# Kernel tuning notes

Measured on AMD Instinct MI355X. Metric: run time of the kernel, lower is better.

Reference implementation:

```python
import jax, jax.numpy as jnp
import numpy as np

N_NODES = 50000


def sage_conv(x, src, dst, Wl, bl, Wr):
    # mean-aggregate neighbor features: message from src -> dst
    msg = x[src]                                            # [E, d]
    agg = jax.ops.segment_sum(msg, dst, num_segments=N_NODES)
    deg = jax.ops.segment_sum(jnp.ones((src.shape[0],), x.dtype), dst,
                              num_segments=N_NODES)
    mean = agg / jnp.clip(deg, 1.0)[:, None]                # [N, d]
    # PyG SAGEConv: lin_l(mean) + lin_r(x); lin_l has bias, lin_r does not
    return mean @ Wl.T + bl + x @ Wr.T


def setup_inputs() -> dict:
    key = jax.random.key(0)
    ks = jax.random.split(key, 10)
    d_in, d_h = 128, 256
    E = 800000
    x = jax.random.normal(ks[0], (N_NODES, d_in), jnp.float32)
    edge_index = jax.random.randint(ks[1], (2, E), 0, N_NODES, jnp.int32)
    s = 0.05
    return {
        "x": x,
        "edge_index": edge_index,
        "W1_l": jax.random.normal(ks[2], (d_h, d_in), jnp.float32) * s,
        "b1": jax.random.normal(ks[3], (d_h,), jnp.float32) * s,
        "W1_r": jax.random.normal(ks[4], (d_h, d_in), jnp.float32) * s,
        "W2_l": jax.random.normal(ks[5], (d_h, d_h), jnp.float32) * s,
        "b2": jax.random.normal(ks[6], (d_h,), jnp.float32) * s,
        "W2_r": jax.random.normal(ks[7], (d_h, d_h), jnp.float32) * s,
        "head_w": jax.random.normal(ks[8], (1, d_h), jnp.float32) * s,
        "head_b": jax.random.normal(ks[9], (1,), jnp.float32) * s,
    }


def reference(x, edge_index, W1_l, b1, W1_r, W2_l, b2, W2_r, head_w, head_b):
    src, dst = edge_index[0], edge_index[1]
    h = jax.nn.relu(sage_conv(x, src, dst, W1_l, b1, W1_r))
    # dropout is identity in eval mode
    h = jax.nn.relu(sage_conv(h, src, dst, W2_l, b2, W2_r))
    out = h @ head_w.T + head_b                              # [N, 1]
    return out[:, 0]                                         # [N]
```

## Files before the change

kernel.cpp:

```cpp
#include <hip/hip_runtime.h>
#include <hip/hip_bf16.h>
#include <hip/hip_fp8.h>

#define D_IN 128
#define D_H  256

typedef __attribute__((ext_vector_type(8))) short short8;
typedef __attribute__((ext_vector_type(4))) float floatx4;

__device__ __forceinline__ unsigned short f2bf(float f) {
    __hip_bfloat16 h = __float2bfloat16(f);
    return *reinterpret_cast<unsigned short*>(&h);
}
__device__ __forceinline__ float bf2f(unsigned short s) {
    union { unsigned int u; float f; } v;
    v.u = ((unsigned int)s) << 16;
    return v.f;
}
__device__ __forceinline__ unsigned char f2fp8(float f) {
    __hip_fp8_e4m3 t(f);
    return (unsigned char)t.__x;
}

__global__ void hist_conv_k(const int* __restrict__ dst, int* __restrict__ deg,
                            int* __restrict__ rank, int E,
                            const float* __restrict__ x, unsigned short* __restrict__ xb,
                            unsigned char* __restrict__ xb8, int nx4,
                            const float* __restrict__ w1l, unsigned short* __restrict__ w1lb,
                            const float* __restrict__ w1r, unsigned short* __restrict__ w1rb, int nw14,
                            const float* __restrict__ w2l, unsigned short* __restrict__ w2lb,
                            const float* __restrict__ w2r, unsigned short* __restrict__ w2rb, int nw24) {
    if (blockIdx.x < 512) {
        for (int e = blockIdx.x * 256 + threadIdx.x; e < E; e += 512 * 256)
            rank[e] = atomicAdd(&deg[dst[e]], 1);
        return;
    }
    int i = (blockIdx.x - 512) * 256 + threadIdx.x;
    if (i < nx4) {
        float4 v = ((const float4*)x)[i];
        ushort4 u;
        u.x = f2bf(v.x); u.y = f2bf(v.y); u.z = f2bf(v.z); u.w = f2bf(v.w);
        ((ushort4*)xb)[i] = u;
        uchar4 c;
        c.x = f2fp8(v.x); c.y = f2fp8(v.y); c.z = f2fp8(v.z); c.w = f2fp8(v.w);
        ((uchar4*)xb8)[i] = c;
        return;
    }
    i -= nx4;
    const float* s; unsigned short* d; int k;
    if (i < nw14) { s = w1l; d = w1lb; k = i; }
    else {
        i -= nw14;
        if (i < nw14) { s = w1r; d = w1rb; k = i; }
        else {
            i -= nw14;
            if (i < nw24) { s = w2l; d = w2lb; k = i; }
            else {
                i -= nw24;
                if (i >= nw24) return;
                s = w2r; d = w2rb; k = i;
            }
        }
    }
    float4 v = ((const float4*)s)[k];
    ushort4 u;
    u.x = f2bf(v.x); u.y = f2bf(v.y); u.z = f2bf(v.z); u.w = f2bf(v.w);
    ((ushort4*)d)[k] = u;
}

__global__ __launch_bounds__(256) void scan_part_k(const int* __restrict__ deg,
                                                   int* __restrict__ bsum, int n) {
    const int b = blockIdx.x, tid = threadIdx.x;
    const int base = b * 2048;
    const int lim = min(base + 2048, n);
    int s = 0;
    for (int i = base + tid; i < lim; i += 256) s += deg[i];
    __shared__ int red[256];
    red[tid] = s; __syncthreads();
    for (int off = 128; off > 0; off >>= 1) {
        if (tid < off) red[tid] += red[tid + off];
        __syncthreads();
    }
    if (tid == 0) bsum[b] = red[0];
}

__global__ __launch_bounds__(256) void scan_final_k(const int* __restrict__ deg,
                                                    const int* __restrict__ bsum,
                                                    int* __restrict__ row_ptr,
                                                    int n, int E) {
    const int b = blockIdx.x, tid = threadIdx.x;
    const int base = b * 2048;
    __shared__ int buf[2048];
    __shared__ int ts[256];
    __shared__ int blk_prefix;
    if (tid == 0) {
        int p = 0;
        for (int i = 0; i < b; ++i) p += bsum[i];
        blk_prefix = p;
    }
    for (int i = tid; i < 2048; i += 256)
        buf[i] = (base + i < n) ? deg[base + i] : 0;
    __syncthreads();
    int local[8];
    int s = 0;
#pragma unroll
    for (int j = 0; j < 8; ++j) { local[j] = s; s += buf[tid * 8 + j]; }
    ts[tid] = s; __syncthreads();
    for (int off = 1; off < 256; off <<= 1) {
        int v = (tid >= off) ? ts[tid - off] : 0;
        __syncthreads();
        ts[tid] += v;
        __syncthreads();
    }
    const int prefix = blk_prefix + ((tid == 0) ? 0 : ts[tid - 1]);
#pragma unroll
    for (int j = 0; j < 8; ++j) {
        int idx = base + tid * 8 + j;
        if (idx < n) row_ptr[idx] = prefix + local[j];
    }
    if (b == 0 && tid == 0) row_ptr[n] = E;
}

__global__ void scatter_k(const int* __restrict__ src, const int* __restrict__ dst,
                          const int* __restrict__ rank, const int* __restrict__ row_ptr,
                          int* __restrict__ col, int E) {
    for (int e = blockIdx.x * blockDim.x + threadIdx.x; e < E; e += gridDim.x * blockDim.x)
        col[row_ptr[dst[e]] + rank[e]] = src[e];
}

template <int UNP>
__device__ __forceinline__ int agg1_stage(const unsigned char* __restrict__ X8,
                                          const int* __restrict__ col,
                                          int j, int e, int sel, int l32, float* acc) {
    for (; j + 2 * UNP <= e; j += 2 * UNP) {
        int c0[UNP], c1[UNP];
#pragma unroll
        for (int u = 0; u < UNP; ++u) { c0[u] = col[j + 2 * u]; c1[u] = col[j + 2 * u + 1]; }
        unsigned int vals[UNP];
#pragma unroll
        for (int u = 0; u < UNP; ++u) {
            const int cs = sel ? c1[u] : c0[u];
            vals[u] = *(const unsigned int*)(X8 + (size_t)cs * 128 + l32 * 4);
        }
#pragma unroll
        for (int u = 0; u < UNP; ++u) {
            __hip_fp8x4_e4m3 p;
            p.__x = vals[u];
            float4 f = (float4)p;
            acc[0] += f.x; acc[1] += f.y; acc[2] += f.z; acc[3] += f.w;
        }
    }
    return j;
}

__global__ __launch_bounds__(256) void aggregate1_k(
    const unsigned char* __restrict__ X8, const int* __restrict__ col,
    const int* __restrict__ rp, unsigned short* __restrict__ out, int Mnodes) {
    int node = __builtin_amdgcn_readfirstlane((blockIdx.x << 2) + (threadIdx.x >> 6));
    if (node >= Mnodes) return;
    const int lane = threadIdx.x & 63;
    const int sel = lane >> 5;
    const int l32 = lane & 31;
    const int s = rp[node], e = rp[node + 1];
    float acc[4] = {0.f, 0.f, 0.f, 0.f};

    int j = s;
    j = agg1_stage<4>(X8, col, j, e, sel, l32, acc);
    j = agg1_stage<2>(X8, col, j, e, sel, l32, acc);
    j = agg1_stage<1>(X8, col, j, e, sel, l32, acc);
    if (j < e) {
        const int c0 = col[j];
        if (sel == 0) {
            unsigned int v = *(const unsigned int*)(X8 + (size_t)c0 * 128 + l32 * 4);
            __hip_fp8x4_e4m3 p;
            p.__x = v;
            float4 f = (float4)p;
            acc[0] += f.x; acc[1] += f.y; acc[2] += f.z; acc[3] += f.w;
        }
    }
#pragma unroll
    for (int k = 0; k < 4; ++k) acc[k] += __shfl_xor(acc[k], 32, 64);
    const float inv = 1.f / fmaxf((float)(e - s), 1.f);
    if (sel == 0) {
        ushort4 o;
        o.x = f2bf(acc[0] * inv); o.y = f2bf(acc[1] * inv);
        o.z = f2bf(acc[2] * inv); o.w = f2bf(acc[3] * inv);
        *(ushort4*)(out + (size_t)node * 128 + l32 * 4) = o;
    }
}

template <int UN>
__device__ __forceinline__ int agg_stage_fp8(const unsigned char* __restrict__ X8,
                                             const int* __restrict__ col,
                                             int j, int e, int lane, float* acc) {
    for (; j + UN <= e; j += UN) {
        int cs[UN];
#pragma unroll
        for (int u = 0; u < UN; ++u) cs[u] = col[j + u];
        unsigned int vals[UN];
#pragma unroll
        for (int u = 0; u < UN; ++u)
            vals[u] = *(const unsigned int*)(X8 + (size_t)cs[u] * 256 + lane * 4);
#pragma unroll
        for (int u = 0; u < UN; ++u) {
            __hip_fp8x4_e4m3 p;
            p.__x = vals[u];
            float4 f = (float4)p;
            acc[0] += f.x; acc[1] += f.y; acc[2] += f.z; acc[3] += f.w;
        }
    }
    return j;
}

__global__ __launch_bounds__(256) void aggregate2_k(
    const unsigned char* __restrict__ X8, const int* __restrict__ col,
    const int* __restrict__ rp, unsigned short* __restrict__ out, int Mnodes) {
    int node = __builtin_amdgcn_readfirstlane((blockIdx.x << 2) + (threadIdx.x >> 6));
    if (node >= Mnodes) return;
    const int lane = threadIdx.x & 63;
    const int s = rp[node], e = rp[node + 1];
    float acc[4] = {0.f, 0.f, 0.f, 0.f};

    int j = s;
    j = agg_stage_fp8<8>(X8, col, j, e, lane, acc);
    j = agg_stage_fp8<4>(X8, col, j, e, lane, acc);
    j = agg_stage_fp8<2>(X8, col, j, e, lane, acc);
    j = agg_stage_fp8<1>(X8, col, j, e, lane, acc);

    const float inv = 1.f / fmaxf((float)(e - s), 1.f);
    ushort4 o;
    o.x = f2bf(acc[0] * inv); o.y = f2bf(acc[1] * inv);
    o.z = f2bf(acc[2] * inv); o.w = f2bf(acc[3] * inv);
    *(ushort4*)(out + (size_t)node * 256 + lane * 4) = o;
}

template <int K, bool HEAD>
__global__ __launch_bounds__(256, 2) void gemm_mfma_k(
    const unsigned short* __restrict__ A1, const unsigned short* __restrict__ W1,
    const unsigned short* __restrict__ A2, const unsigned short* __restrict__ W2,
    const float* __restrict__ bias, unsigned short* __restrict__ Hout,
    unsigned char* __restrict__ Hout8,
    const float* __restrict__ hw, const float* __restrict__ hb,
    float* __restrict__ out, int M) {
    __shared__ __align__(16) unsigned short sA[128 * 40];
    __shared__ __align__(16) unsigned short sB[256 * 40];
    __shared__ float head_acc[128];

    constexpr int NCK = K / 32;
    constexpr int NC = 2 * NCK;

    const int tid = threadIdx.x;
    const int wave = tid >> 6;
    const int lane = tid & 63;
    const int c = lane & 15;
    const int q = lane >> 4;
    const int m0 = blockIdx.x * 128;

    if (HEAD && tid < 128) head_acc[tid] = 0.f;

    floatx4 acc[8][4];
#pragma unroll
    for (int mi = 0; mi < 8; ++mi)
#pragma unroll
        for (int ni = 0; ni < 4; ++ni) acc[mi][ni] = (floatx4){0.f, 0.f, 0.f, 0.f};

    const int arow = tid >> 1;
    const int aseg = (tid & 1) * 16;
    const int brow = tid >> 2;
    const int bseg = (tid & 3) * 8;
    int gr = m0 + arow;
    if (gr >= M) gr = M - 1;

    auto loadChunk = [&](int t, short8& a0, short8& a1, short8* b) {
        const unsigned short* Ap = (t >= NCK) ? A2 : A1;
        const unsigned short* Wp = (t >= NCK) ? W2 : W1;
        const int k0 = (t & (NCK - 1)) * 32;
        a0 = *(const short8*)(Ap + (size_t)gr * K + k0 + aseg);
        a1 = *(const short8*)(Ap + (size_t)gr * K + k0 + aseg + 8);
#pragma unroll
        for (int i = 0; i < 4; ++i)
            b[i] = *(const short8*)(Wp + (size_t)(brow + i * 64) * K + k0 + bseg);
    };

    short8 ca0, ca1, cb[4], na0, na1, nb[4];
    loadChunk(0, ca0, ca1, cb);

#pragma unroll 1
    for (int t = 0; t < NC; ++t) {
        __syncthreads();
        *(short8*)&sA[arow * 40 + aseg] = ca0;
        *(short8*)&sA[arow * 40 + aseg + 8] = ca1;
#pragma unroll
        for (int i = 0; i < 4; ++i)
            *(short8*)&sB[(brow + i * 64) * 40 + bseg] = cb[i];
        if (t + 1 < NC)
            loadChunk(t + 1, na0, na1, nb);
        __syncthreads();

        short8 af[8], bf[4];
#pragma unroll
        for (int mi = 0; mi < 8; ++mi)
            af[mi] = *(const short8*)&sA[(mi * 16 + c) * 40 + q * 8];
#pragma unroll
        for (int ni = 0; ni < 4; ++ni)
            bf[ni] = *(const short8*)&sB[(wave * 64 + ni * 16 + c) * 40 + q * 8];
#pragma unroll
        for (int mi = 0; mi < 8; ++mi)
#pragma unroll
            for (int ni = 0; ni < 4; ++ni)
                acc[mi][ni] = __builtin_amdgcn_mfma_f32_16x16x32_bf16(
                    af[mi], bf[ni], acc[mi][ni], 0, 0, 0);

        ca0 = na0; ca1 = na1;
#pragma unroll
        for (int i = 0; i < 4; ++i) cb[i] = nb[i];
    }

    if (!HEAD) {
#pragma unroll
        for (int mi = 0; mi < 8; ++mi)
#pragma unroll
            for (int ni = 0; ni < 4; ++ni) {
                const int n = wave * 64 + ni * 16 + c;
                const float bv = bias[n];
#pragma unroll
                for (int reg = 0; reg < 4; ++reg) {
                    const int m = m0 + mi * 16 + q * 4 + reg;
                    if (m < M) {
                        float v = fmaxf(acc[mi][ni][reg] + bv, 0.f);
                        Hout[(size_t)m * 256 + n] = f2bf(v);
                        Hout8[(size_t)m * 256 + n] = f2fp8(v);
                    }
                }
            }
    } else {
#pragma unroll
        for (int mi = 0; mi < 8; ++mi) {
            float p[4] = {0.f, 0.f, 0.f, 0.f};
#pragma unroll
            for (int ni = 0; ni < 4; ++ni) {
                const int n = wave * 64 + ni * 16 + c;
                const float bv = bias[n];
                const float hv = hw[n];
#pragma unroll
                for (int reg = 0; reg < 4; ++reg)
                    p[reg] += fmaxf(acc[mi][ni][reg] + bv, 0.f) * hv;
            }
#pragma unroll
            for (int reg = 0; reg < 4; ++reg) {
                float v = p[reg];
                v += __shfl_xor(v, 1, 64);
                v += __shfl_xor(v, 2, 64);
                v += __shfl_xor(v, 4, 64);
                v += __shfl_xor(v, 8, 64);
                if (c == 0) atomicAdd(&head_acc[mi * 16 + q * 4 + reg], v);
            }
        }
        __syncthreads();
        if (tid < 128) {
            const int m = m0 + tid;
            if (m < M) out[m] = head_acc[tid] + hb[0];
        }
    }
}

extern "C" void kernel_launch(void* const* d_in, const int* in_sizes, int n_in,
                              void* d_out, int out_size, void* d_ws, size_t ws_size,
                              hipStream_t stream) {
    const float* x    = (const float*)d_in[0];
    const int*   ei   = (const int*)d_in[1];
    const float* W1l  = (const float*)d_in[2];
    const float* b1   = (const float*)d_in[3];
    const float* W1r  = (const float*)d_in[4];
    const float* W2l  = (const float*)d_in[5];
    const float* b2   = (const float*)d_in[6];
    const float* W2r  = (const float*)d_in[7];
    const float* hw   = (const float*)d_in[8];
    const float* hb   = (const float*)d_in[9];
    float* out = (float*)d_out;

    const int M = in_sizes[0] / D_IN;
    const int E = in_sizes[1] / 2;
    const int* src = ei;
    const int* dst = ei + E;

    size_t off = 0;
    auto alloc = [&](size_t bytes) -> void* {
        void* p = (char*)d_ws + off;
        off += (bytes + 255) & ~(size_t)255;
        return p;
    };
    int* deg  = (int*)alloc((size_t)M * 4);
    int* rp   = (int*)alloc((size_t)(M + 1) * 4);
    int* bsum = (int*)alloc(256 * 4);
    int* rank = (int*)alloc((size_t)E * 4);
    int* col  = (int*)alloc((size_t)E * 4);
    unsigned short* xb    = (unsigned short*)alloc((size_t)M * D_IN * 2);
    unsigned char*  xb8   = (unsigned char*)alloc((size_t)M * D_IN);
    unsigned short* w1lb  = (unsigned short*)alloc((size_t)D_H * D_IN * 2);
    unsigned short* w1rb  = (unsigned short*)alloc((size_t)D_H * D_IN * 2);
    unsigned short* w2lb  = (unsigned short*)alloc((size_t)D_H * D_H * 2);
    unsigned short* w2rb  = (unsigned short*)alloc((size_t)D_H * D_H * 2);
    unsigned short* mean1 = (unsigned short*)alloc((size_t)M * D_IN * 2);
    unsigned short* h1    = (unsigned short*)alloc((size_t)M * D_H * 2);
    unsigned char*  h8    = (unsigned char*)alloc((size_t)M * D_H);
    unsigned short* mean2 = (unsigned short*)alloc((size_t)M * D_H * 2);

    hipMemsetAsync(deg, 0, (size_t)M * 4, stream);

    const int nx4 = (M * D_IN) / 4;
    const int nw14 = (D_H * D_IN) / 4;
    const int nw24 = (D_H * D_H) / 4;
    const int tot4 = nx4 + 2 * nw14 + 2 * nw24;
    const int convblk = (tot4 + 255) / 256;
    hist_conv_k<<<512 + convblk, 256, 0, stream>>>(
        dst, deg, rank, E,
        x, xb, xb8, nx4, W1l, w1lb, W1r, w1rb, nw14, W2l, w2lb, W2r, w2rb, nw24);

    const int nseg = (M + 2047) / 2048;
    scan_part_k<<<nseg, 256, 0, stream>>>(deg, bsum, M);
    scan_final_k<<<nseg, 256, 0, stream>>>(deg, bsum, rp, M, E);
    scatter_k<<<512, 256, 0, stream>>>(src, dst, rank, rp, col, E);

    const int nblk = (M + 127) / 128;
    const int ablk = (M + 3) / 4;

    aggregate1_k<<<ablk, 256, 0, stream>>>(xb8, col, rp, mean1, M);
    gemm_mfma_k<D_IN, false><<<nblk, 256, 0, stream>>>(
        mean1, w1lb, xb, w1rb, b1, h1, h8, nullptr, nullptr, nullptr, M);

    aggregate2_k<<<ablk, 256, 0, stream>>>(h8, col, rp, mean2, M);
    gemm_mfma_k<D_H, true><<<nblk, 256, 0, stream>>>(
        mean2, w2lb, h1, w2rb, b2, nullptr, nullptr, hw, hb, out, M);
}
```

Measured before the change: 247.1 us.

## Replace global-atomic CSR build with two-level bucket sort using LDS histograms

Builds the destination-sorted CSR in two passes. The first pass histograms edges into 128-node buckets with per-block shared-memory counters and scatters packed (local dst, src) words into bucket-contiguous staging. A per-bucket kernel then counts, scans and places edges within its bucket in LDS. This removes the 800K global atomics on deg, the rank array and the memset, in exchange for more kernel launches and an extra staging pass. Packing src into 16 bits assumes node ids stay below 65536, and edge order within a node becomes nondeterministic.

```diff
diff --git a/kernel.cpp b/kernel.cpp
--- a/kernel.cpp
+++ b/kernel.cpp
@@ -4,6 +4,9 @@
 
 #define D_IN 128
 #define D_H  256
+#define NBLK 128
+#define BSH  7
+#define BNODES 128
 
 typedef __attribute__((ext_vector_type(8))) short short8;
 typedef __attribute__((ext_vector_type(4))) float floatx4;
@@ -22,20 +25,26 @@
     return (unsigned char)t.__x;
 }
 
-__global__ void hist_conv_k(const int* __restrict__ dst, int* __restrict__ deg,
-                            int* __restrict__ rank, int E,
-                            const float* __restrict__ x, unsigned short* __restrict__ xb,
-                            unsigned char* __restrict__ xb8, int nx4,
-                            const float* __restrict__ w1l, unsigned short* __restrict__ w1lb,
-                            const float* __restrict__ w1r, unsigned short* __restrict__ w1rb, int nw14,
-                            const float* __restrict__ w2l, unsigned short* __restrict__ w2lb,
-                            const float* __restrict__ w2r, unsigned short* __restrict__ w2rb, int nw24) {
-    if (blockIdx.x < 512) {
-        for (int e = blockIdx.x * 256 + threadIdx.x; e < E; e += 512 * 256)
-            rank[e] = atomicAdd(&deg[dst[e]], 1);
+__global__ void p1_hist_conv_k(const int* __restrict__ dst, int* __restrict__ cnt2d,
+                               int E, int NB,
+                               const float* __restrict__ x, unsigned short* __restrict__ xb,
+                               unsigned char* __restrict__ xb8, int nx4,
+                               const float* __restrict__ w1l, unsigned short* __restrict__ w1lb,
+                               const float* __restrict__ w1r, unsigned short* __restrict__ w1rb, int nw14,
+                               const float* __restrict__ w2l, unsigned short* __restrict__ w2lb,
+                               const float* __restrict__ w2r, unsigned short* __restrict__ w2rb, int nw24) {
+    if (blockIdx.x < NBLK) {
+        __shared__ int h[512];
+        for (int i = threadIdx.x; i < NB; i += 256) h[i] = 0;
+        __syncthreads();
+        for (int e = blockIdx.x * 256 + threadIdx.x; e < E; e += NBLK * 256)
+            atomicAdd(&h[dst[e] >> BSH], 1);
+        __syncthreads();
+        for (int i = threadIdx.x; i < NB; i += 256)
+            cnt2d[blockIdx.x * NB + i] = h[i];
         return;
     }
-    int i = (blockIdx.x - 512) * 256 + threadIdx.x;
+    int i = (blockIdx.x - NBLK) * 256 + threadIdx.x;
     if (i < nx4) {
         float4 v = ((const float4*)x)[i];
         ushort4 u;
@@ -68,64 +77,96 @@
     ((ushort4*)d)[k] = u;
 }
 
-__global__ __launch_bounds__(256) void scan_part_k(const int* __restrict__ deg,
-                                                   int* __restrict__ bsum, int n) {
-    const int b = blockIdx.x, tid = threadIdx.x;
-    const int base = b * 2048;
-    const int lim = min(base + 2048, n);
-    int s = 0;
-    for (int i = base + tid; i < lim; i += 256) s += deg[i];
-    __shared__ int red[256];
-    red[tid] = s; __syncthreads();
-    for (int off = 128; off > 0; off >>= 1) {
-        if (tid < off) red[tid] += red[tid + off];
-        __syncthreads();
-    }
-    if (tid == 0) bsum[b] = red[0];
-}
-
-__global__ __launch_bounds__(256) void scan_final_k(const int* __restrict__ deg,
-                                                    const int* __restrict__ bsum,
-                                                    int* __restrict__ row_ptr,
-                                                    int n, int E) {
-    const int b = blockIdx.x, tid = threadIdx.x;
-    const int base = b * 2048;
-    __shared__ int buf[2048];
-    __shared__ int ts[256];
-    __shared__ int blk_prefix;
-    if (tid == 0) {
-        int p = 0;
-        for (int i = 0; i < b; ++i) p += bsum[i];
-        blk_prefix = p;
-    }
-    for (int i = tid; i < 2048; i += 256)
-        buf[i] = (base + i < n) ? deg[base + i] : 0;
-    __syncthreads();
-    int local[8];
-    int s = 0;
-#pragma unroll
-    for (int j = 0; j < 8; ++j) { local[j] = s; s += buf[tid * 8 + j]; }
-    ts[tid] = s; __syncthreads();
-    for (int off = 1; off < 256; off <<= 1) {
-        int v = (tid >= off) ? ts[tid - off] : 0;
-        __syncthreads();
-        ts[tid] += v;
-        __syncthreads();
-    }
-    const int prefix = blk_prefix + ((tid == 0) ? 0 : ts[tid - 1]);
-#pragma unroll
-    for (int j = 0; j < 8; ++j) {
-        int idx = base + tid * 8 + j;
-        if (idx < n) row_ptr[idx] = prefix + local[j];
-    }
-    if (b == 0 && tid == 0) row_ptr[n] = E;
-}
-
-__global__ void scatter_k(const int* __restrict__ src, const int* __restrict__ dst,
-                          const int* __restrict__ rank, const int* __restrict__ row_ptr,
-                          int* __restrict__ col, int E) {
-    for (int e = blockIdx.x * blockDim.x + threadIdx.x; e < E; e += gridDim.x * blockDim.x)
-        col[row_ptr[dst[e]] + rank[e]] = src[e];
+__global__ __launch_bounds__(NBLK) void bucket_scan_k(const int* __restrict__ cnt2d,
+                                                      int* __restrict__ off2d,
+                                                      int* __restrict__ tot, int NB) {
+    const int B = blockIdx.x, t = threadIdx.x;
+    __shared__ int sc[NBLK];
+    __shared__ int orig[NBLK];
+    int v = cnt2d[t * NB + B];
+    orig[t] = v; sc[t] = v;
+    __syncthreads();
+    for (int off = 1; off < NBLK; off <<= 1) {
+        int u = (t >= off) ? sc[t - off] : 0;
+        __syncthreads();
+        sc[t] += u;
+        __syncthreads();
+    }
+    off2d[t * NB + B] = sc[t] - orig[t];
+    if (t == NBLK - 1) tot[B] = sc[t];
+}
+
+__global__ __launch_bounds__(512) void base_scan_k(const int* __restrict__ tot,
+                                                   int* __restrict__ base,
+                                                   int* __restrict__ rp,
+                                                   int NB, int M, int E) {
+    __shared__ int sc[512];
+    const int t = threadIdx.x;
+    int v = (t < NB) ? tot[t] : 0;
+    sc[t] = v;
+    __syncthreads();
+    for (int off = 1; off < 512; off <<= 1) {
+        int u = (t >= off) ? sc[t - off] : 0;
+        __syncthreads();
+        sc[t] += u;
+        __syncthreads();
+    }
+    if (t < NB) base[t] = sc[t] - v;
+    if (t == NB - 1) base[NB] = sc[t];
+    if (t == 0) rp[M] = E;
+}
+
+__global__ __launch_bounds__(256) void place_k(const int* __restrict__ src,
+                                               const int* __restrict__ dst,
+                                               const int* __restrict__ off2d,
+                                               const int* __restrict__ base,
+                                               unsigned int* __restrict__ staging,
+                                               int E, int NB) {
+    __shared__ int cur[512];
+    const int b = blockIdx.x;
+    for (int i = threadIdx.x; i < NB; i += 256)
+        cur[i] = base[i] + off2d[b * NB + i];
+    __syncthreads();
+    for (int e = b * 256 + threadIdx.x; e < E; e += NBLK * 256) {
+        const int d = dst[e];
+        const int pos = atomicAdd(&cur[d >> BSH], 1);
+        staging[pos] = ((unsigned int)(d & (BNODES - 1)) << 16) | (unsigned int)src[e];
+    }
+}
+
+__global__ __launch_bounds__(256) void bucket_sort_k(const unsigned int* __restrict__ staging,
+                                                     const int* __restrict__ base,
+                                                     int* __restrict__ rp, int* __restrict__ col,
+                                                     int M) {
+    const int B = blockIdx.x, tid = threadIdx.x;
+    __shared__ int h[BNODES], sc[BNODES], cur[BNODES];
+    if (tid < BNODES) h[tid] = 0;
+    __syncthreads();
+    const int s0 = base[B], s1 = base[B + 1];
+    for (int i = s0 + tid; i < s1; i += 256)
+        atomicAdd(&h[staging[i] >> 16], 1);
+    __syncthreads();
+    if (tid < BNODES) sc[tid] = h[tid];
+    __syncthreads();
+    for (int off = 1; off < BNODES; off <<= 1) {
+        int v = 0;
+        if (tid < BNODES && tid >= off) v = sc[tid - off];
+        __syncthreads();
+        if (tid < BNODES) sc[tid] += v;
+        __syncthreads();
+    }
+    if (tid < BNODES) {
+        const int excl = sc[tid] - h[tid];
+        const int node = B * BNODES + tid;
+        if (node < M) rp[node] = s0 + excl;
+        cur[tid] = s0 + excl;
+    }
+    __syncthreads();
+    for (int i = s0 + tid; i < s1; i += 256) {
+        const unsigned int u = staging[i];
+        const int pos = atomicAdd(&cur[u >> 16], 1);
+        col[pos] = (int)(u & 0xFFFFu);
+    }
 }
 
 template <int UNP>
@@ -383,6 +424,7 @@
     const int E = in_sizes[1] / 2;
     const int* src = ei;
     const int* dst = ei + E;
+    const int NB = (M + BNODES - 1) / BNODES;
 
     size_t off = 0;
     auto alloc = [&](size_t bytes) -> void* {
@@ -390,11 +432,13 @@
         off += (bytes + 255) & ~(size_t)255;
         return p;
     };
-    int* deg  = (int*)alloc((size_t)M * 4);
-    int* rp   = (int*)alloc((size_t)(M + 1) * 4);
-    int* bsum = (int*)alloc(256 * 4);
-    int* rank = (int*)alloc((size_t)E * 4);
-    int* col  = (int*)alloc((size_t)E * 4);
+    int* cnt2d = (int*)alloc((size_t)NBLK * NB * 4);
+    int* off2d = (int*)alloc((size_t)NBLK * NB * 4);
+    int* tot   = (int*)alloc((size_t)NB * 4);
+    int* base  = (int*)alloc((size_t)(NB + 1) * 4);
+    unsigned int* staging = (unsigned int*)alloc((size_t)E * 4);
+    int* rp    = (int*)alloc((size_t)(M + 1) * 4);
+    int* col   = (int*)alloc((size_t)E * 4);
     unsigned short* xb    = (unsigned short*)alloc((size_t)M * D_IN * 2);
     unsigned char*  xb8   = (unsigned char*)alloc((size_t)M * D_IN);
     unsigned short* w1lb  = (unsigned short*)alloc((size_t)D_H * D_IN * 2);
@@ -406,21 +450,18 @@
     unsigned char*  h8    = (unsigned char*)alloc((size_t)M * D_H);
     unsigned short* mean2 = (unsigned short*)alloc((size_t)M * D_H * 2);
 
-    hipMemsetAsync(deg, 0, (size_t)M * 4, stream);
-
     const int nx4 = (M * D_IN) / 4;
     const int nw14 = (D_H * D_IN) / 4;
     const int nw24 = (D_H * D_H) / 4;
     const int tot4 = nx4 + 2 * nw14 + 2 * nw24;
     const int convblk = (tot4 + 255) / 256;
-    hist_conv_k<<<512 + convblk, 256, 0, stream>>>(
-        dst, deg, rank, E,
+    p1_hist_conv_k<<<NBLK + convblk, 256, 0, stream>>>(
+        dst, cnt2d, E, NB,
         x, xb, xb8, nx4, W1l, w1lb, W1r, w1rb, nw14, W2l, w2lb, W2r, w2rb, nw24);
-
-    const int nseg = (M + 2047) / 2048;
-    scan_part_k<<<nseg, 256, 0, stream>>>(deg, bsum, M);
-    scan_final_k<<<nseg, 256, 0, stream>>>(deg, bsum, rp, M, E);
-    scatter_k<<<512, 256, 0, stream>>>(src, dst, rank, rp, col, E);
+    bucket_scan_k<<<NB, NBLK, 0, stream>>>(cnt2d, off2d, tot, NB);
+    base_scan_k<<<1, 512, 0, stream>>>(tot, base, rp, NB, M, E);
+    place_k<<<NBLK, 256, 0, stream>>>(src, dst, off2d, base, staging, E, NB);
+    bucket_sort_k<<<NB, 256, 0, stream>>>(staging, base, rp, col, M);
 
     const int nblk = (M + 127) / 128;
     const int ablk = (M + 3) / 4;
```

Result: faster. 232.8 us (-5.8%).
